# Performance work log

Hardware: AMD Instinct MI355X
Metric: run time of the kernel (lower is better)

The kernel has to match this reference:

```python
import jax, jax.numpy as jnp
import numpy as np

B, T, D, H, O = 8, 16384, 256, 256, 256


def setup_inputs() -> dict:
    key = jax.random.key(0)
    ks = jax.random.split(key, 7)
    lim_d = 1.0 / np.sqrt(D)
    lim_h = 1.0 / np.sqrt(H)
    u = lambda k, shape, lim: jax.random.uniform(k, shape, jnp.float32, -lim, lim)
    return {
        "xs": jax.random.normal(ks[0], (B, T, D), jnp.float32),
        "Wz": u(ks[1], (H, D), lim_d),
        "bz": u(ks[2], (H,), lim_d),
        "Wh": u(ks[3], (H, D), lim_d),
        "bh": u(ks[4], (H,), lim_d),
        "Wo": u(ks[5], (O, H), lim_h),
        "bo": u(ks[6], (O,), lim_h),
    }


def reference(xs, Wz, bz, Wh, bh, Wo, bo):
    # gates and candidate hidden states (eqx.nn.Linear: y = W @ x + b)
    zs = jax.nn.sigmoid(jnp.einsum("btd,hd->bth", xs, Wz) + bz)  # [B,T,H]
    hs = jnp.einsum("btd,hd->bth", xs, Wh) + bh                  # [B,T,H]

    # prepend_ones / prepend_zeros along the time axis
    a = jnp.concatenate([jnp.ones_like(zs[:, :1]), 1.0 - zs], axis=1)    # [B,T+1,H]
    b = jnp.concatenate([jnp.zeros_like(zs[:, :1]), zs * hs], axis=1)    # [B,T+1,H]

    def combine(first, second):
        a0, b0 = first
        a1, b1 = second
        return (a0 * b0, b0 * a1 + b1)

    _, states = jax.lax.associative_scan(combine, (a, b), axis=1)
    return jnp.einsum("bth,oh->bto", states[:, 1:], Wo) + bo  # [B,T,O]
```

## Files before the change

### kernel.cpp

```cpp
#include <hip/hip_runtime.h>
#include <hip/hip_bf16.h>

#define Bsz 8
#define Tsz 16384
#define NL0 16385
#define NL5 512
#define NL10 16

typedef __attribute__((ext_vector_type(2))) float f32x2;
typedef __attribute__((ext_vector_type(4))) float f32x4;
typedef __attribute__((ext_vector_type(8))) short bf16x8;

__device__ __forceinline__ short f2bf(float f) {
  unsigned u = __builtin_bit_cast(unsigned, f);
  u += 0x7FFFu + ((u >> 16) & 1u);
  return (short)(u >> 16);
}
__device__ __forceinline__ unsigned cvtpk(float lo, float hi) {
  __hip_bfloat162 t = __float22bfloat162_rn(float2{lo, hi});
  unsigned u;
  __builtin_memcpy(&u, &t, 4);
  return u;
}
__device__ __forceinline__ bf16x8 pack8(f32x4 a, f32x4 b) {
  union { unsigned u[4]; bf16x8 v; } r;
  r.u[0] = cvtpk(a[0], a[1]); r.u[1] = cvtpk(a[2], a[3]);
  r.u[2] = cvtpk(b[0], b[1]); r.u[3] = cvtpk(b[2], b[3]);
  return r.v;
}
__device__ __forceinline__ void unpk(unsigned u, float& a, float& b) {
  a = __builtin_bit_cast(float, u << 16);
  b = __builtin_bit_cast(float, u & 0xFFFF0000u);
}

__global__ void fill_sentinel(float* __restrict__ out, int n) {
  int i = blockIdx.x * blockDim.x + threadIdx.x;
  if (i < n) out[i] = 12345.0f;
}

__global__ void prep_weights(const float* __restrict__ Wz, const float* __restrict__ Wh,
                             const float* __restrict__ Wo, unsigned short* __restrict__ wt) {
  int idx = blockIdx.x * 256 + threadIdx.x;
  if (idx >= 3 * 256 * 32) return;
  int m   = idx >> 13;
  int rem = idx & 8191;
  int r   = rem >> 5;
  int cq  = rem & 31;
  const float* src = (m == 0 ? Wz : (m == 1 ? Wh : Wo)) + r * 256 + cq * 8;
  f32x4 v0 = *(const f32x4*)src;
  f32x4 v1 = *(const f32x4*)(src + 4);
  *(bf16x8*)(wt + m * 65536 + (cq * 256 + r) * 8) = pack8(v0, v1);
}

__global__ __launch_bounds__(256, 3)
void gemm_zh(const float* __restrict__ xs, const unsigned short* __restrict__ wt,
             const float* __restrict__ bz, const float* __restrict__ bh,
             unsigned* __restrict__ l0, f32x2* __restrict__ l5)
{
  __shared__ __align__(16) unsigned short aL[32][32][8];

  const int tid = threadIdx.x;
  const int wave = tid >> 6, lane = tid & 63, l15 = lane & 15, l4 = lane >> 4;
  const int bid = blockIdx.x;
  const int batch = bid / 513;
  const int cb = bid - batch * 513;
  const long gr0 = (long)batch * Tsz + 32L * cb - 1;
  const unsigned short* wz_t = wt;
  const unsigned short* wh_t = wt + 65536;
  const int wn = wave * 64;

  {
    f32x4 av0[4], av1[4];
#pragma unroll
    for (int k = 0; k < 4; ++k) {
      const int row = (tid >> 5) + k * 8;
      const int col = (tid & 31) * 8;
      long gr = gr0 + row;
      gr = gr < 0 ? 0 : (gr > (long)Bsz * Tsz - 1 ? (long)Bsz * Tsz - 1 : gr);
      const float* p = xs + gr * 256 + col;
      av0[k] = *(const f32x4*)p;
      av1[k] = *(const f32x4*)(p + 4);
    }
#pragma unroll
    for (int k = 0; k < 4; ++k) {
      const int o = tid + k * 256;
      const int row = o >> 5, oct = o & 31;
      *(bf16x8*)&aL[row][oct ^ (row & 7)][0] = pack8(av0[k], av1[k]);
    }
  }
  __syncthreads();

  f32x4 accz[2][4] = {};
  f32x4 acch[2][4] = {};

#pragma unroll
  for (int kk = 0; kk < 8; ++kk) {
    bf16x8 af[2];
#pragma unroll
    for (int m = 0; m < 2; ++m) {
      const int row = m * 16 + l15;
      af[m] = *(const bf16x8*)&aL[row][(kk * 4 + l4) ^ (row & 7)][0];
    }
    const int cq = kk * 4 + l4;
    bf16x8 zf[4], hf[4];
#pragma unroll
    for (int n = 0; n < 4; ++n) {
      const int r = wn + n * 16 + l15;
      zf[n] = *(const bf16x8*)(wz_t + (cq * 256 + r) * 8);
      hf[n] = *(const bf16x8*)(wh_t + (cq * 256 + r) * 8);
    }
#pragma unroll
    for (int m = 0; m < 2; ++m)
#pragma unroll
      for (int n = 0; n < 4; ++n) {
        accz[m][n] = __builtin_amdgcn_mfma_f32_16x16x32_bf16(af[m], zf[n], accz[m][n], 0, 0, 0);
        acch[m][n] = __builtin_amdgcn_mfma_f32_16x16x32_bf16(af[m], hf[n], acch[m][n], 0, 0, 0);
      }
  }

  const int idx0 = 32 * cb;
#pragma unroll
  for (int n = 0; n < 4; ++n) {
    const int col = wn + n * 16 + l15;
    const float bzv = bz[col], bhv = bh[col];
#pragma unroll
    for (int m = 0; m < 2; ++m)
#pragma unroll
      for (int j = 0; j < 4; ++j) {
        const int e = m * 16 + l4 * 4 + j;
        const float zv = 1.0f / (1.0f + __expf(-(accz[m][n][j] + bzv)));
        const float hv = acch[m][n][j] + bhv;
        float a = 1.0f - zv, b = zv * hv;
        if (cb == 0 && e == 0) { a = 1.0f; b = 0.0f; }
        const unsigned u = cvtpk(a, b);
        if (cb < 512 || e == 0)
          l0[((size_t)batch * NL0 + idx0 + e) * 256 + col] = u;
        float ar, br; unpk(u, ar, br);
        accz[m][n][j] = ar; acch[m][n][j] = br;
      }
  }

  if (cb < 512) {
    const bool f3 = (l4 & 1) == 0;
    const bool f4 = (l4 & 2) == 0;
#pragma unroll
    for (int n = 0; n < 4; ++n) {
      float a4v[2], b4v[2];
#pragma unroll
      for (int m = 0; m < 2; ++m) {
        const float a10 = accz[m][n][0] * acch[m][n][0];
        const float b10 = acch[m][n][0] * accz[m][n][1] + acch[m][n][1];
        const float a11 = accz[m][n][2] * acch[m][n][2];
        const float b11 = acch[m][n][2] * accz[m][n][3] + acch[m][n][3];
        const float a2 = a10 * b10;
        const float b2 = b10 * a11 + b11;
        const float pa = __shfl_xor(a2, 16);
        const float pb = __shfl_xor(b2, 16);
        const float a3 = f3 ? a2 * b2 : pa * pb;
        const float b3 = f3 ? b2 * pa + pb : pb * a2 + b2;
        const float qa = __shfl_xor(a3, 32);
        const float qb = __shfl_xor(b3, 32);
        a4v[m] = f4 ? a3 * b3 : qa * qb;
        b4v[m] = f4 ? b3 * qa + qb : qb * a3 + b3;
      }
      const float a5 = a4v[0] * b4v[0];
      const float b5 = b4v[0] * a4v[1] + b4v[1];
      if (l4 == 0)
        l5[((size_t)batch * 512 + cb) * 256 + wn + n * 16 + l15] = f32x2{a5, b5};
    }
  }
}

__global__ __launch_bounds__(256)
void chunk_up(const f32x2* __restrict__ src, f32x2* __restrict__ dst, int nCh, int nSrc)
{
  int idx = blockIdx.x * 256 + threadIdx.x;
  int total = Bsz * nCh * 256;
  if (idx >= total) return;
  int h = idx & 255, r = idx >> 8;
  int c = r % nCh, batch = r / nCh;
  size_t base = ((size_t)batch * nSrc + (size_t)c * 32) * 256 + h;

  float a1[16], b1[16];
#pragma unroll
  for (int i = 0; i < 16; ++i) {
    f32x2 e0 = src[base + (size_t)(2 * i) * 256];
    f32x2 e1 = src[base + (size_t)(2 * i + 1) * 256];
    a1[i] = e0[0] * e0[1];
    b1[i] = e0[1] * e1[0] + e1[1];
  }
#pragma unroll
  for (int n = 8; n >= 1; n >>= 1) {
#pragma unroll
    for (int i = 0; i < n; ++i) {
      float na = a1[2 * i] * b1[2 * i];
      float nb = b1[2 * i] * a1[2 * i + 1] + b1[2 * i + 1];
      a1[i] = na; b1[i] = nb;
    }
  }
  dst[((size_t)batch * nCh + c) * 256 + h] = f32x2{a1[0], b1[0]};
}

__global__ void tree16(const f32x2* __restrict__ src, float* __restrict__ outB)
{
  int idx = blockIdx.x * 256 + threadIdx.x;
  if (idx >= Bsz * 256) return;
  int h = idx & 255, batch = idx >> 8;
  size_t base = (size_t)batch * 16 * 256 + h;

  float a0[16], b0[16];
#pragma unroll
  for (int i = 0; i < 16; ++i) { f32x2 e = src[base + (size_t)i * 256]; a0[i] = e[0]; b0[i] = e[1]; }
  float a1[8], b1[8];
#pragma unroll
  for (int i = 0; i < 8; ++i) { a1[i] = a0[2*i]*b0[2*i]; b1[i] = b0[2*i]*a0[2*i+1] + b0[2*i+1]; }
  float a2[4], b2[4];
#pragma unroll
  for (int i = 0; i < 4; ++i) { a2[i] = a1[2*i]*b1[2*i]; b2[i] = b1[2*i]*a1[2*i+1] + b1[2*i+1]; }
  float a3[2], b3[2];
#pragma unroll
  for (int i = 0; i < 2; ++i) { a3[i] = a2[2*i]*b2[2*i]; b3[i] = b2[2*i]*a2[2*i+1] + b2[2*i+1]; }
  float s3[2];
  s3[0] = b3[0];
  s3[1] = b3[0] * a3[1] + b3[1];
  float s2[4];
  s2[0] = b2[0]; s2[1] = s3[0]; s2[2] = s3[0] * a2[2] + b2[2]; s2[3] = s3[1];
  float s1[8];
  s1[0] = b1[0];
#pragma unroll
  for (int j = 0; j < 4; ++j) s1[2*j+1] = s2[j];
#pragma unroll
  for (int j = 1; j < 4; ++j) s1[2*j] = s2[j-1] * a1[2*j] + b1[2*j];
  float s0[16];
  s0[0] = b0[0];
#pragma unroll
  for (int j = 0; j < 8; ++j) s0[2*j+1] = s1[j];
#pragma unroll
  for (int j = 1; j < 8; ++j) s0[2*j] = s1[j-1] * a0[2*j] + b0[2*j];
#pragma unroll
  for (int i = 0; i < 16; ++i) outB[base + (size_t)i * 256] = s0[i];
}

__global__ __launch_bounds__(256, 2)
void chunk_down_f32(const f32x2* __restrict__ src, const float* __restrict__ snext,
                    float* __restrict__ outF, int nCh, int nFull, int nSrc)
{
  int idx = blockIdx.x * 256 + threadIdx.x;
  int total = Bsz * nCh * 256;
  if (idx >= total) return;
  int h = idx & 255, r = idx >> 8;
  int c = r % nCh, batch = r / nCh;
  size_t base = ((size_t)batch * nSrc + (size_t)c * 32) * 256 + h;
  bool hasP = (c > 0);
  float P = hasP ? snext[((size_t)batch * nFull + (c - 1)) * 256 + h] : 0.0f;
  float S = snext[((size_t)batch * nFull + c) * 256 + h];

  float ae[16], be[16], a1[16], b1[16];
#pragma unroll
  for (int i = 0; i < 16; ++i) {
    f32x2 e0 = src[base + (size_t)(2 * i) * 256];
    f32x2 e1 = src[base + (size_t)(2 * i + 1) * 256];
    ae[i] = e0[0]; be[i] = e0[1];
    a1[i] = e0[0] * e0[1];
    b1[i] = e0[1] * e1[0] + e1[1];
  }
  float a2[8], b2[8];
#pragma unroll
  for (int i = 0; i < 8; ++i) { a2[i] = a1[2*i]*b1[2*i]; b2[i] = b1[2*i]*a1[2*i+1] + b1[2*i+1]; }
  float a3[4], b3[4];
#pragma unroll
  for (int i = 0; i < 4; ++i) { a3[i] = a2[2*i]*b2[2*i]; b3[i] = b2[2*i]*a2[2*i+1] + b2[2*i+1]; }
  float a4[2], b4[2];
#pragma unroll
  for (int i = 0; i < 2; ++i) { a4[i] = a3[2*i]*b3[2*i]; b4[i] = b3[2*i]*a3[2*i+1] + b3[2*i+1]; }

  float s4[2];
  s4[0] = hasP ? P * a4[0] + b4[0] : b4[0];
  s4[1] = S;
  float s3[4];
  s3[0] = hasP ? P * a3[0] + b3[0] : b3[0];
  s3[1] = s4[0]; s3[2] = s4[0] * a3[2] + b3[2]; s3[3] = s4[1];
  float s2[8];
  s2[0] = hasP ? P * a2[0] + b2[0] : b2[0];
#pragma unroll
  for (int j = 0; j < 4; ++j) s2[2*j+1] = s3[j];
#pragma unroll
  for (int j = 1; j < 4; ++j) s2[2*j] = s3[j-1] * a2[2*j] + b2[2*j];
  float s1[16];
  s1[0] = hasP ? P * a1[0] + b1[0] : b1[0];
#pragma unroll
  for (int j = 0; j < 8; ++j) s1[2*j+1] = s2[j];
#pragma unroll
  for (int j = 1; j < 8; ++j) s1[2*j] = s2[j-1] * a1[2*j] + b1[2*j];

  outF[base] = hasP ? P * ae[0] + be[0] : be[0];
#pragma unroll
  for (int j = 0; j < 16; ++j) outF[base + (size_t)(2*j+1) * 256] = s1[j];
#pragma unroll
  for (int j = 1; j < 16; ++j) outF[base + (size_t)(2*j) * 256] = s1[j-1] * ae[j] + be[j];
}

__global__ __launch_bounds__(256, 2)
void down_proj(const unsigned* __restrict__ l0, const float* __restrict__ s5b,
               const unsigned short* __restrict__ wo_t, const float* __restrict__ bo,
               float* __restrict__ out)
{
  __shared__ unsigned short pL[32 * 256];

  const int tid = threadIdx.x;
  const int bc = blockIdx.x;
  const int c = bc % 513;
  const int batch = bc / 513;

  {
    const int h = tid;
    const size_t base = ((size_t)batch * NL0 + (size_t)c * 32) * 256 + h;
    const bool hasP = (c > 0);
    const float P = hasP ? s5b[((size_t)batch * 512 + (c - 1)) * 256 + h] : 0.0f;

    if (c == 512) {
      float a0, b0; unpk(l0[base], a0, b0);
      pL[h] = (unsigned short)f2bf(P * a0 + b0);
#pragma unroll
      for (int i = 1; i < 32; ++i)
        pL[i * 256 + (h ^ ((i & 7) << 3))] = 0;
    } else {
      const float S = s5b[((size_t)batch * 512 + c) * 256 + h];
      float ae[16], be[16], a1[16], b1[16];
#pragma unroll
      for (int i = 0; i < 16; ++i) {
        unsigned u0 = l0[base + (size_t)(2 * i) * 256];
        unsigned u1 = l0[base + (size_t)(2 * i + 1) * 256];
        float a0, b0, a1e, b1e;
        unpk(u0, a0, b0); unpk(u1, a1e, b1e);
        ae[i] = a0; be[i] = b0;
        a1[i] = a0 * b0; b1[i] = b0 * a1e + b1e;
      }
      float a2[8], b2[8];
#pragma unroll
      for (int i = 0; i < 8; ++i) { a2[i] = a1[2*i]*b1[2*i]; b2[i] = b1[2*i]*a1[2*i+1] + b1[2*i+1]; }
      float a3[4], b3[4];
#pragma unroll
      for (int i = 0; i < 4; ++i) { a3[i] = a2[2*i]*b2[2*i]; b3[i] = b2[2*i]*a2[2*i+1] + b2[2*i+1]; }
      float a4[2], b4[2];
#pragma unroll
      for (int i = 0; i < 2; ++i) { a4[i] = a3[2*i]*b3[2*i]; b4[i] = b3[2*i]*a3[2*i+1] + b3[2*i+1]; }

      float s4[2];
      s4[0] = hasP ? P * a4[0] + b4[0] : b4[0];
      s4[1] = S;
      float s3[4];
      s3[0] = hasP ? P * a3[0] + b3[0] : b3[0];
      s3[1] = s4[0]; s3[2] = s4[0] * a3[2] + b3[2]; s3[3] = s4[1];
      float s2[8];
      s2[0] = hasP ? P * a2[0] + b2[0] : b2[0];
#pragma unroll
      for (int j = 0; j < 4; ++j) s2[2*j+1] = s3[j];
#pragma unroll
      for (int j = 1; j < 4; ++j) s2[2*j] = s3[j-1] * a2[2*j] + b2[2*j];
      float s1[16];
      s1[0] = hasP ? P * a1[0] + b1[0] : b1[0];
#pragma unroll
      for (int j = 0; j < 8; ++j) s1[2*j+1] = s2[j];
#pragma unroll
      for (int j = 1; j < 8; ++j) s1[2*j] = s2[j-1] * a1[2*j] + b1[2*j];

      pL[h] = (unsigned short)f2bf(hasP ? P * ae[0] + be[0] : be[0]);
#pragma unroll
      for (int j = 0; j < 16; ++j) {
        const int row = 2 * j + 1;
        pL[row * 256 + (h ^ ((row & 7) << 3))] = (unsigned short)f2bf(s1[j]);
      }
#pragma unroll
      for (int j = 1; j < 16; ++j) {
        const int row = 2 * j;
        pL[row * 256 + (h ^ ((row & 7) << 3))] = (unsigned short)f2bf(s1[j-1] * ae[j] + be[j]);
      }
    }
  }
  __syncthreads();

  const int wave = tid >> 6, lane = tid & 63, l15 = lane & 15, l4 = lane >> 4;
  const int wn = wave * 64;
  f32x4 acc[2][4] = {};
  bf16x8 wc[4], wnx[4];
#pragma unroll
  for (int n = 0; n < 4; ++n)
    wc[n] = *(const bf16x8*)(wo_t + (l4 * 256 + wn + n * 16 + l15) * 8);
#pragma unroll
  for (int kk = 0; kk < 8; ++kk) {
    if (kk < 7) {
#pragma unroll
      for (int n = 0; n < 4; ++n)
        wnx[n] = *(const bf16x8*)(wo_t + (((kk + 1) * 4 + l4) * 256 + wn + n * 16 + l15) * 8);
    }
    bf16x8 af[2];
#pragma unroll
    for (int m = 0; m < 2; ++m) {
      const int row = m * 16 + l15;
      af[m] = *(const bf16x8*)&pL[row * 256 + ((kk * 32 + l4 * 8) ^ ((row & 7) << 3))];
    }
#pragma unroll
    for (int m = 0; m < 2; ++m)
#pragma unroll
      for (int n = 0; n < 4; ++n)
        acc[m][n] = __builtin_amdgcn_mfma_f32_16x16x32_bf16(af[m], wc[n], acc[m][n], 0, 0, 0);
    if (kk < 7) {
      wc[0] = wnx[0]; wc[1] = wnx[1]; wc[2] = wnx[2]; wc[3] = wnx[3];
    }
  }

  const int tBase = 32 * c - 1;
#pragma unroll
  for (int n = 0; n < 4; ++n) {
    const int col = wn + n * 16 + l15;
    const float bv = bo[col];
#pragma unroll
    for (int m = 0; m < 2; ++m)
#pragma unroll
      for (int j = 0; j < 4; ++j) {
        const int t = tBase + m * 16 + l4 * 4 + j;
        if ((unsigned)t < (unsigned)Tsz)
          out[((size_t)batch * Tsz + t) * 256 + col] = acc[m][n][j] + bv;
      }
  }
}

extern "C" void kernel_launch(void* const* d_in, const int* in_sizes, int n_in,
                              void* d_out, int out_size, void* d_ws, size_t ws_size,
                              hipStream_t stream)
{
  (void)in_sizes; (void)n_in;
  const float* xs = (const float*)d_in[0];
  const float* Wz = (const float*)d_in[1];
  const float* bz = (const float*)d_in[2];
  const float* Wh = (const float*)d_in[3];
  const float* bh = (const float*)d_in[4];
  const float* Wo = (const float*)d_in[5];
  const float* bo = (const float*)d_in[6];
  float* out = (float*)d_out;

  const size_t n_l0  = (size_t)Bsz * NL0 * 256;
  const size_t n_l5  = (size_t)Bsz * NL5 * 256;
  const size_t n_l10 = (size_t)Bsz * NL10 * 256;

  unsigned* l0    = (unsigned*)d_ws;
  f32x2* l5ab     = (f32x2*)(l0 + n_l0);
  f32x2* l10ab    = l5ab + n_l5;
  float* s10b     = (float*)(l10ab + n_l10);
  float* s5b      = s10b + n_l10;
  unsigned short* wt = (unsigned short*)(s5b + n_l5);

  const size_t need = n_l0 * 4 + n_l5 * 8 + n_l10 * 8 + n_l10 * 4 + n_l5 * 4 + 3 * 65536 * 2;
  if (ws_size < need) {
    fill_sentinel<<<(out_size + 255) / 256, 256, 0, stream>>>(out, out_size);
    return;
  }

  prep_weights<<<96, 256, 0, stream>>>(Wz, Wh, Wo, wt);
  gemm_zh<<<Bsz * 513, 256, 0, stream>>>(xs, wt, bz, bh, l0, l5ab);

  chunk_up<<<(Bsz * 16 * 256) / 256, 256, 0, stream>>>(l5ab, l10ab, 16, NL5);
  tree16<<<8, 256, 0, stream>>>(l10ab, s10b);
  chunk_down_f32<<<(Bsz * 16 * 256) / 256, 256, 0, stream>>>(l5ab, s10b, s5b, 16, 16, NL5);

  down_proj<<<Bsz * 513, 256, 0, stream>>>(l0, s5b, wt + 2 * 65536, bo, out);
}
```

Measured before the change: 171.6 us.

## Fuse three mid-level scan kernels into one per-batch kernel and use 32-bit indexing

Replaces the chunk_up, tree16 and chunk_down_f32 launches with a single mid_scan kernel, one block per batch, that reduces the 16 chunks, scans them in registers and propagates back down. This removes two kernel launches and the global round trip for the level-10 intermediates. In exchange the middle stage now runs on only 8 blocks with serial loops over chunks, so it has much less parallelism. Index math in gemm_zh and down_proj also switches from 64-bit to per-batch-based 32-bit offsets to trim address arithmetic.

```diff
diff --git a/kernel.cpp b/kernel.cpp
--- a/kernel.cpp
+++ b/kernel.cpp
@@ -5,7 +5,6 @@
 #define Tsz 16384
 #define NL0 16385
 #define NL5 512
-#define NL10 16
 
 typedef __attribute__((ext_vector_type(2))) float f32x2;
 typedef __attribute__((ext_vector_type(4))) float f32x4;
@@ -64,20 +63,24 @@
   const int bid = blockIdx.x;
   const int batch = bid / 513;
   const int cb = bid - batch * 513;
-  const long gr0 = (long)batch * Tsz + 32L * cb - 1;
   const unsigned short* wz_t = wt;
   const unsigned short* wh_t = wt + 65536;
   const int wn = wave * 64;
 
+  unsigned* const l0b = l0 + (size_t)batch * (NL0 * 256);
+  f32x2* const l5b = l5 + (size_t)batch * (512 * 256);
+
   {
+    const int gr0i = batch * Tsz + 32 * cb - 1;
+    const int rowsMax = Bsz * Tsz - 1;
     f32x4 av0[4], av1[4];
 #pragma unroll
     for (int k = 0; k < 4; ++k) {
       const int row = (tid >> 5) + k * 8;
       const int col = (tid & 31) * 8;
-      long gr = gr0 + row;
-      gr = gr < 0 ? 0 : (gr > (long)Bsz * Tsz - 1 ? (long)Bsz * Tsz - 1 : gr);
-      const float* p = xs + gr * 256 + col;
+      int gr = gr0i + row;
+      gr = gr < 0 ? 0 : (gr > rowsMax ? rowsMax : gr);
+      const float* p = xs + (((unsigned)gr << 8) + (unsigned)col);
       av0[k] = *(const f32x4*)p;
       av1[k] = *(const f32x4*)(p + 4);
     }
@@ -118,7 +121,7 @@
       }
   }
 
-  const int idx0 = 32 * cb;
+  const unsigned base0 = ((unsigned)(32 * cb) << 8) + (unsigned)(wn + l15) + ((unsigned)l4 << 10);
 #pragma unroll
   for (int n = 0; n < 4; ++n) {
     const int col = wn + n * 16 + l15;
@@ -134,7 +137,7 @@
         if (cb == 0 && e == 0) { a = 1.0f; b = 0.0f; }
         const unsigned u = cvtpk(a, b);
         if (cb < 512 || e == 0)
-          l0[((size_t)batch * NL0 + idx0 + e) * 256 + col] = u;
+          l0b[base0 + (unsigned)(n * 16 + m * 4096 + j * 256)] = u;
         float ar, br; unpk(u, ar, br);
         accz[m][n][j] = ar; acch[m][n][j] = br;
       }
@@ -166,138 +169,121 @@
       const float a5 = a4v[0] * b4v[0];
       const float b5 = b4v[0] * a4v[1] + b4v[1];
       if (l4 == 0)
-        l5[((size_t)batch * 512 + cb) * 256 + wn + n * 16 + l15] = f32x2{a5, b5};
+        l5b[((unsigned)cb << 8) + (unsigned)(wn + n * 16 + l15)] = f32x2{a5, b5};
     }
   }
 }
 
 __global__ __launch_bounds__(256)
-void chunk_up(const f32x2* __restrict__ src, f32x2* __restrict__ dst, int nCh, int nSrc)
+void mid_scan(const f32x2* __restrict__ l5, float* __restrict__ s5b)
 {
-  int idx = blockIdx.x * 256 + threadIdx.x;
-  int total = Bsz * nCh * 256;
-  if (idx >= total) return;
-  int h = idx & 255, r = idx >> 8;
-  int c = r % nCh, batch = r / nCh;
-  size_t base = ((size_t)batch * nSrc + (size_t)c * 32) * 256 + h;
-
-  float a1[16], b1[16];
-#pragma unroll
-  for (int i = 0; i < 16; ++i) {
-    f32x2 e0 = src[base + (size_t)(2 * i) * 256];
-    f32x2 e1 = src[base + (size_t)(2 * i + 1) * 256];
-    a1[i] = e0[0] * e0[1];
-    b1[i] = e0[1] * e1[0] + e1[1];
-  }
-#pragma unroll
-  for (int n = 8; n >= 1; n >>= 1) {
-#pragma unroll
-    for (int i = 0; i < n; ++i) {
-      float na = a1[2 * i] * b1[2 * i];
-      float nb = b1[2 * i] * a1[2 * i + 1] + b1[2 * i + 1];
-      a1[i] = na; b1[i] = nb;
-    }
-  }
-  dst[((size_t)batch * nCh + c) * 256 + h] = f32x2{a1[0], b1[0]};
-}
-
-__global__ void tree16(const f32x2* __restrict__ src, float* __restrict__ outB)
-{
-  int idx = blockIdx.x * 256 + threadIdx.x;
-  if (idx >= Bsz * 256) return;
-  int h = idx & 255, batch = idx >> 8;
-  size_t base = (size_t)batch * 16 * 256 + h;
-
-  float a0[16], b0[16];
-#pragma unroll
-  for (int i = 0; i < 16; ++i) { f32x2 e = src[base + (size_t)i * 256]; a0[i] = e[0]; b0[i] = e[1]; }
-  float a1[8], b1[8];
-#pragma unroll
-  for (int i = 0; i < 8; ++i) { a1[i] = a0[2*i]*b0[2*i]; b1[i] = b0[2*i]*a0[2*i+1] + b0[2*i+1]; }
-  float a2[4], b2[4];
-#pragma unroll
-  for (int i = 0; i < 4; ++i) { a2[i] = a1[2*i]*b1[2*i]; b2[i] = b1[2*i]*a1[2*i+1] + b1[2*i+1]; }
-  float a3[2], b3[2];
-#pragma unroll
-  for (int i = 0; i < 2; ++i) { a3[i] = a2[2*i]*b2[2*i]; b3[i] = b2[2*i]*a2[2*i+1] + b2[2*i+1]; }
-  float s3[2];
-  s3[0] = b3[0];
-  s3[1] = b3[0] * a3[1] + b3[1];
-  float s2[4];
-  s2[0] = b2[0]; s2[1] = s3[0]; s2[2] = s3[0] * a2[2] + b2[2]; s2[3] = s3[1];
-  float s1[8];
-  s1[0] = b1[0];
-#pragma unroll
-  for (int j = 0; j < 4; ++j) s1[2*j+1] = s2[j];
-#pragma unroll
-  for (int j = 1; j < 4; ++j) s1[2*j] = s2[j-1] * a1[2*j] + b1[2*j];
-  float s0[16];
-  s0[0] = b0[0];
-#pragma unroll
-  for (int j = 0; j < 8; ++j) s0[2*j+1] = s1[j];
-#pragma unroll
-  for (int j = 1; j < 8; ++j) s0[2*j] = s1[j-1] * a0[2*j] + b0[2*j];
-#pragma unroll
-  for (int i = 0; i < 16; ++i) outB[base + (size_t)i * 256] = s0[i];
-}
-
-__global__ __launch_bounds__(256, 2)
-void chunk_down_f32(const f32x2* __restrict__ src, const float* __restrict__ snext,
-                    float* __restrict__ outF, int nCh, int nFull, int nSrc)
-{
-  int idx = blockIdx.x * 256 + threadIdx.x;
-  int total = Bsz * nCh * 256;
-  if (idx >= total) return;
-  int h = idx & 255, r = idx >> 8;
-  int c = r % nCh, batch = r / nCh;
-  size_t base = ((size_t)batch * nSrc + (size_t)c * 32) * 256 + h;
-  bool hasP = (c > 0);
-  float P = hasP ? snext[((size_t)batch * nFull + (c - 1)) * 256 + h] : 0.0f;
-  float S = snext[((size_t)batch * nFull + c) * 256 + h];
-
-  float ae[16], be[16], a1[16], b1[16];
-#pragma unroll
-  for (int i = 0; i < 16; ++i) {
-    f32x2 e0 = src[base + (size_t)(2 * i) * 256];
-    f32x2 e1 = src[base + (size_t)(2 * i + 1) * 256];
-    ae[i] = e0[0]; be[i] = e0[1];
-    a1[i] = e0[0] * e0[1];
-    b1[i] = e0[1] * e1[0] + e1[1];
-  }
-  float a2[8], b2[8];
-#pragma unroll
-  for (int i = 0; i < 8; ++i) { a2[i] = a1[2*i]*b1[2*i]; b2[i] = b1[2*i]*a1[2*i+1] + b1[2*i+1]; }
-  float a3[4], b3[4];
-#pragma unroll
-  for (int i = 0; i < 4; ++i) { a3[i] = a2[2*i]*b2[2*i]; b3[i] = b2[2*i]*a2[2*i+1] + b2[2*i+1]; }
-  float a4[2], b4[2];
-#pragma unroll
-  for (int i = 0; i < 2; ++i) { a4[i] = a3[2*i]*b3[2*i]; b4[i] = b3[2*i]*a3[2*i+1] + b3[2*i+1]; }
-
-  float s4[2];
-  s4[0] = hasP ? P * a4[0] + b4[0] : b4[0];
-  s4[1] = S;
-  float s3[4];
-  s3[0] = hasP ? P * a3[0] + b3[0] : b3[0];
-  s3[1] = s4[0]; s3[2] = s4[0] * a3[2] + b3[2]; s3[3] = s4[1];
-  float s2[8];
-  s2[0] = hasP ? P * a2[0] + b2[0] : b2[0];
-#pragma unroll
-  for (int j = 0; j < 4; ++j) s2[2*j+1] = s3[j];
-#pragma unroll
-  for (int j = 1; j < 4; ++j) s2[2*j] = s3[j-1] * a2[2*j] + b2[2*j];
-  float s1[16];
-  s1[0] = hasP ? P * a1[0] + b1[0] : b1[0];
-#pragma unroll
-  for (int j = 0; j < 8; ++j) s1[2*j+1] = s2[j];
-#pragma unroll
-  for (int j = 1; j < 8; ++j) s1[2*j] = s2[j-1] * a1[2*j] + b1[2*j];
-
-  outF[base] = hasP ? P * ae[0] + be[0] : be[0];
-#pragma unroll
-  for (int j = 0; j < 16; ++j) outF[base + (size_t)(2*j+1) * 256] = s1[j];
-#pragma unroll
-  for (int j = 1; j < 16; ++j) outF[base + (size_t)(2*j) * 256] = s1[j-1] * ae[j] + be[j];
+  const int batch = blockIdx.x;
+  const int h = threadIdx.x;
+  const f32x2* src = l5 + (size_t)batch * (512 * 256) + h;
+  float* dst = s5b + (size_t)batch * (512 * 256) + h;
+
+  float la[16], lb[16];
+#pragma unroll 1
+  for (int c = 0; c < 16; ++c) {
+    float a1[16], b1[16];
+#pragma unroll
+    for (int i = 0; i < 16; ++i) {
+      f32x2 e0 = src[(unsigned)(c * 32 + 2 * i) << 8];
+      f32x2 e1 = src[(unsigned)(c * 32 + 2 * i + 1) << 8];
+      a1[i] = e0[0] * e0[1];
+      b1[i] = e0[1] * e1[0] + e1[1];
+    }
+#pragma unroll
+    for (int n = 8; n >= 1; n >>= 1)
+#pragma unroll
+      for (int i = 0; i < n; ++i) {
+        float na = a1[2 * i] * b1[2 * i];
+        float nb = b1[2 * i] * a1[2 * i + 1] + b1[2 * i + 1];
+        a1[i] = na; b1[i] = nb;
+      }
+    la[c] = a1[0]; lb[c] = b1[0];
+  }
+
+  float s10[16];
+  {
+    float a1[8], b1[8];
+#pragma unroll
+    for (int i = 0; i < 8; ++i) { a1[i] = la[2*i]*lb[2*i]; b1[i] = lb[2*i]*la[2*i+1] + lb[2*i+1]; }
+    float a2[4], b2[4];
+#pragma unroll
+    for (int i = 0; i < 4; ++i) { a2[i] = a1[2*i]*b1[2*i]; b2[i] = b1[2*i]*a1[2*i+1] + b1[2*i+1]; }
+    float a3[2], b3[2];
+#pragma unroll
+    for (int i = 0; i < 2; ++i) { a3[i] = a2[2*i]*b2[2*i]; b3[i] = b2[2*i]*a2[2*i+1] + b2[2*i+1]; }
+    float s3[2];
+    s3[0] = b3[0];
+    s3[1] = b3[0] * a3[1] + b3[1];
+    float s2[4];
+    s2[0] = b2[0]; s2[1] = s3[0]; s2[2] = s3[0] * a2[2] + b2[2]; s2[3] = s3[1];
+    float s1[8];
+    s1[0] = b1[0];
+#pragma unroll
+    for (int j = 0; j < 4; ++j) s1[2*j+1] = s2[j];
+#pragma unroll
+    for (int j = 1; j < 4; ++j) s1[2*j] = s2[j-1] * a1[2*j] + b1[2*j];
+    s10[0] = lb[0];
+#pragma unroll
+    for (int j = 0; j < 8; ++j) s10[2*j+1] = s1[j];
+#pragma unroll
+    for (int j = 1; j < 8; ++j) s10[2*j] = s1[j-1] * la[2*j] + lb[2*j];
+  }
+
+#pragma unroll 1
+  for (int c = 0; c < 16; ++c) {
+    const bool hasP = (c > 0);
+    const float P = hasP ? s10[c - 1] : 0.0f;
+    const float S = s10[c];
+    const unsigned cbase = (unsigned)(c * 32) << 8;
+
+    float ae[16], be[16], a1[16], b1[16];
+#pragma unroll
+    for (int i = 0; i < 16; ++i) {
+      f32x2 e0 = src[cbase + ((unsigned)(2 * i) << 8)];
+      f32x2 e1 = src[cbase + ((unsigned)(2 * i + 1) << 8)];
+      ae[i] = e0[0]; be[i] = e0[1];
+      a1[i] = e0[0] * e0[1];
+      b1[i] = e0[1] * e1[0] + e1[1];
+    }
+    float a2[8], b2[8];
+#pragma unroll
+    for (int i = 0; i < 8; ++i) { a2[i] = a1[2*i]*b1[2*i]; b2[i] = b1[2*i]*a1[2*i+1] + b1[2*i+1]; }
+    float a3[4], b3[4];
+#pragma unroll
+    for (int i = 0; i < 4; ++i) { a3[i] = a2[2*i]*b2[2*i]; b3[i] = b2[2*i]*a2[2*i+1] + b2[2*i+1]; }
+    float a4[2], b4[2];
+#pragma unroll
+    for (int i = 0; i < 2; ++i) { a4[i] = a3[2*i]*b3[2*i]; b4[i] = b3[2*i]*a3[2*i+1] + b3[2*i+1]; }
+
+    float s4[2];
+    s4[0] = hasP ? P * a4[0] + b4[0] : b4[0];
+    s4[1] = S;
+    float s3[4];
+    s3[0] = hasP ? P * a3[0] + b3[0] : b3[0];
+    s3[1] = s4[0]; s3[2] = s4[0] * a3[2] + b3[2]; s3[3] = s4[1];
+    float s2[8];
+    s2[0] = hasP ? P * a2[0] + b2[0] : b2[0];
+#pragma unroll
+    for (int j = 0; j < 4; ++j) s2[2*j+1] = s3[j];
+#pragma unroll
+    for (int j = 1; j < 4; ++j) s2[2*j] = s3[j-1] * a2[2*j] + b2[2*j];
+    float s1[16];
+    s1[0] = hasP ? P * a1[0] + b1[0] : b1[0];
+#pragma unroll
+    for (int j = 0; j < 8; ++j) s1[2*j+1] = s2[j];
+#pragma unroll
+    for (int j = 1; j < 8; ++j) s1[2*j] = s2[j-1] * a1[2*j] + b1[2*j];
+
+    dst[cbase] = hasP ? P * ae[0] + be[0] : be[0];
+#pragma unroll
+    for (int j = 0; j < 16; ++j) dst[cbase + ((unsigned)(2*j+1) << 8)] = s1[j];
+#pragma unroll
+    for (int j = 1; j < 16; ++j) dst[cbase + ((unsigned)(2*j) << 8)] = s1[j-1] * ae[j] + be[j];
+  }
 }
 
 __global__ __launch_bounds__(256, 2)
@@ -312,25 +298,29 @@
   const int c = bc % 513;
   const int batch = bc / 513;
 
+  const unsigned* const l0b = l0 + (size_t)batch * (NL0 * 256);
+  const float* const s5bb = s5b + (size_t)batch * (512 * 256);
+  float* const outb = out + (size_t)batch * (Tsz * 256);
+
   {
     const int h = tid;
-    const size_t base = ((size_t)batch * NL0 + (size_t)c * 32) * 256 + h;
+    const unsigned base = ((unsigned)(c * 32) << 8) + (unsigned)h;
     const bool hasP = (c > 0);
-    const float P = hasP ? s5b[((size_t)batch * 512 + (c - 1)) * 256 + h] : 0.0f;
+    const float P = hasP ? s5bb[((unsigned)(c - 1) << 8) + h] : 0.0f;
 
     if (c == 512) {
-      float a0, b0; unpk(l0[base], a0, b0);
+      float a0, b0; unpk(l0b[base], a0, b0);
       pL[h] = (unsigned short)f2bf(P * a0 + b0);
 #pragma unroll
       for (int i = 1; i < 32; ++i)
         pL[i * 256 + (h ^ ((i & 7) << 3))] = 0;
     } else {
-      const float S = s5b[((size_t)batch * 512 + c) * 256 + h];
+      const float S = s5bb[((unsigned)c << 8) + h];
       float ae[16], be[16], a1[16], b1[16];
 #pragma unroll
       for (int i = 0; i < 16; ++i) {
-        unsigned u0 = l0[base + (size_t)(2 * i) * 256];
-        unsigned u1 = l0[base + (size_t)(2 * i + 1) * 256];
+        unsigned u0 = l0b[base + ((unsigned)(2 * i) << 8)];
+        unsigned u1 = l0b[base + ((unsigned)(2 * i + 1) << 8)];
         float a0, b0, a1e, b1e;
         unpk(u0, a0, b0); unpk(u1, a1e, b1e);
         ae[i] = a0; be[i] = b0;
@@ -421,7 +411,7 @@
       for (int j = 0; j < 4; ++j) {
         const int t = tBase + m * 16 + l4 * 4 + j;
         if ((unsigned)t < (unsigned)Tsz)
-          out[((size_t)batch * Tsz + t) * 256 + col] = acc[m][n][j] + bv;
+          outb[((unsigned)t << 8) + (unsigned)col] = acc[m][n][j] + bv;
       }
   }
 }
@@ -440,18 +430,15 @@
   const float* bo = (const float*)d_in[6];
   float* out = (float*)d_out;
 
-  const size_t n_l0  = (size_t)Bsz * NL0 * 256;
-  const size_t n_l5  = (size_t)Bsz * NL5 * 256;
-  const size_t n_l10 = (size_t)Bsz * NL10 * 256;
+  const size_t n_l0 = (size_t)Bsz * NL0 * 256;
+  const size_t n_l5 = (size_t)Bsz * NL5 * 256;
 
   unsigned* l0    = (unsigned*)d_ws;
   f32x2* l5ab     = (f32x2*)(l0 + n_l0);
-  f32x2* l10ab    = l5ab + n_l5;
-  float* s10b     = (float*)(l10ab + n_l10);
-  float* s5b      = s10b + n_l10;
+  float* s5b      = (float*)(l5ab + n_l5);
   unsigned short* wt = (unsigned short*)(s5b + n_l5);
 
-  const size_t need = n_l0 * 4 + n_l5 * 8 + n_l10 * 8 + n_l10 * 4 + n_l5 * 4 + 3 * 65536 * 2;
+  const size_t need = n_l0 * 4 + n_l5 * 8 + n_l5 * 4 + 3 * 65536 * 2;
   if (ws_size < need) {
     fill_sentinel<<<(out_size + 255) / 256, 256, 0, stream>>>(out, out_size);
     return;
@@ -459,10 +446,6 @@
 
   prep_weights<<<96, 256, 0, stream>>>(Wz, Wh, Wo, wt);
   gemm_zh<<<Bsz * 513, 256, 0, stream>>>(xs, wt, bz, bh, l0, l5ab);
-
-  chunk_up<<<(Bsz * 16 * 256) / 256, 256, 0, stream>>>(l5ab, l10ab, 16, NL5);
-  tree16<<<8, 256, 0, stream>>>(l10ab, s10b);
-  chunk_down_f32<<<(Bsz * 16 * 256) / 256, 256, 0, stream>>>(l5ab, s10b, s5b, 16, 16, NL5);
-
+  mid_scan<<<Bsz, 256, 0, stream>>>(l5ab, s5b);
   down_proj<<<Bsz * 513, 256, 0, stream>>>(l0, s5b, wt + 2 * 65536, bo, out);
 }
```

Measured after the change: 194.5 us. 13.3% more time.
